# Optimization experiments

Measured on AMD Instinct MI355X. Metric: run time of the kernel, lower is better.

## Reference

```python
import jax, jax.numpy as jnp
import numpy as np
from jax import lax

TAU = 2.0      # LIF decay constant (source: tau = 2.0)
V_TH = 1.0     # spikingjelly LIFNode default threshold
ALPHA = 2.0    # ATan surrogate default alpha
BN_EPS = 1e-5


@jax.custom_vjp
def spike(v):
    # Heaviside with ATan surrogate gradient (spikingjelly surrogate.ATan)
    return (v >= V_TH).astype(v.dtype)

def _spike_fwd(v):
    return spike(v), v

def _spike_bwd(v, g):
    x = (jnp.pi / 2.0) * ALPHA * (v - V_TH)
    return (g * (ALPHA / 2.0) / (1.0 + x * x),)

spike.defvjp(_spike_fwd, _spike_bwd)


def lif_step(v, x):
    # leaky integrate: v += (x - (v - v_reset)) / tau, v_reset = 0
    v = v + (x - v) / TAU
    s = spike(v)
    # hard reset to 0; detach_reset=True -> stop_gradient on s in the reset path
    v = v * (1.0 - lax.stop_gradient(s))
    return v, s


def multistep_lif(x_seq):
    # x_seq: (T, ...) ; membrane state carried across T, initial v = 0
    v0 = jnp.zeros_like(x_seq[0])
    _, s_seq = lax.scan(lif_step, v0, x_seq)
    return s_seq


def setup_inputs() -> dict:
    key = jax.random.key(0)
    ks = jax.random.split(key, 3)
    bs, length, c_num, hidden = 64, 128, 32, 256
    x = jax.random.normal(ks[0], (bs, length, c_num), dtype=jnp.float32)
    conv_w = jax.random.normal(ks[1], (hidden, 1, 1, 3), dtype=jnp.float32) * 0.3
    conv_b = jnp.zeros((hidden,), jnp.float32)
    bn_gamma = jnp.ones((hidden,), jnp.float32)
    bn_beta = jnp.zeros((hidden,), jnp.float32)
    bn_mean = jnp.zeros((hidden,), jnp.float32)
    bn_var = jnp.ones((hidden,), jnp.float32)
    lin_w = jax.random.normal(ks[2], (hidden, hidden), dtype=jnp.float32) * (1.0 / np.sqrt(hidden))
    lin_b = jnp.zeros((hidden,), jnp.float32)
    return {"x": x, "conv_w": conv_w, "conv_b": conv_b, "bn_gamma": bn_gamma,
            "bn_beta": bn_beta, "bn_mean": bn_mean, "bn_var": bn_var,
            "lin_w": lin_w, "lin_b": lin_b}


def reference(x, conv_w, conv_b, bn_gamma, bn_beta, bn_mean, bn_var, lin_w, lin_b):
    bs, length, c_num = x.shape
    hidden = conv_w.shape[0]

    # ---- ConvEncoder ----
    xi = jnp.transpose(x, (0, 2, 1))[:, None]  # (bs, 1, c_num, length)
    enc = lax.conv_general_dilated(
        xi, conv_w, window_strides=(1, 1), padding=((0, 0), (1, 1)),
        dimension_numbers=("NCHW", "OIHW", "NCHW"))
    enc = enc + conv_b[None, :, None, None]
    # BatchNorm2d (eval mode, running stats)
    inv = bn_gamma * lax.rsqrt(bn_var + BN_EPS)
    enc = (enc - bn_mean[None, :, None, None]) * inv[None, :, None, None] + bn_beta[None, :, None, None]
    # multi-step LIF over channel dim T = hidden (as in source permute(1,0,2,3))
    enc = jnp.transpose(enc, (1, 0, 2, 3))          # (hidden, bs, c_num, length)
    spks_enc = multistep_lif(enc)                   # (hidden, bs, c_num, length)

    # ---- reshape to per-(bs*c_num) sequences of length `length` with feature hidden ----
    h = jnp.transpose(spks_enc, (1, 2, 3, 0)).reshape(bs * c_num, length, hidden)

    # ---- SpikeRNNCell recurrence over time (Linear + stateful LIF) ----
    def rnn_step(v, x_t):                           # x_t: (N, hidden)
        z = x_t @ lin_w.T + lin_b
        v = v + (z - v) / TAU
        s = spike(v)
        v = v * (1.0 - lax.stop_gradient(s))
        return v, s

    v0 = jnp.zeros((bs * c_num, hidden), x.dtype)
    _, s_seq = lax.scan(rnn_step, v0, jnp.transpose(h, (1, 0, 2)))  # (length, N, hidden)
    spks = s_seq[-1]                                # final-step spikes (N, hidden)

    spks = spks.reshape(bs, c_num * hidden, -1)     # (bs, c_num*hidden, 1)
    return jnp.transpose(spks, (0, 2, 1)), spks[:, :, -1]
```

## Files before the change

kernel.cpp:

```cpp
#include <hip/hip_runtime.h>
#include <stdint.h>

typedef unsigned short u16;
typedef unsigned int u32;
typedef unsigned long long u64;
typedef unsigned char u8;

typedef __attribute__((ext_vector_type(4))) int   i32x4;
typedef __attribute__((ext_vector_type(8))) int   i32x8;
typedef __attribute__((ext_vector_type(4))) float f32x4;
typedef __attribute__((ext_vector_type(2))) float f32x2;

#define OFF_WQ4  0u
#define WQ4_BYTES (2u * 32768u)
#define OFF_SCL  (OFF_WQ4 + WQ4_BYTES)

__device__ __forceinline__ f32x2 pk_fma(f32x2 a, f32x2 b, f32x2 c) {
    f32x2 d;
    asm("v_pk_fma_f32 %0, %1, %2, %3"
        : "=v"(d) : "v"(a), "v"(b), "v"(c));
    return d;
}
__device__ __forceinline__ f32x2 pk_fma_lw(f32x2 a, f32x2 b) {
    f32x2 d;
    asm("v_pk_fma_f32 %0, %1, %2, %1 op_sel:[0,0,1] op_sel_hi:[0,1,1]"
        : "=v"(d) : "v"(a), "v"(b));
    return d;
}
__device__ __forceinline__ f32x2 pk_fma_b11(f32x2 a, f32x2 b, f32x2 c) {
    f32x2 d;
    asm("v_pk_fma_f32 %0, %1, %2, %3 op_sel:[1,0,0] op_sel_hi:[1,1,1]"
        : "=v"(d) : "v"(a), "v"(b), "v"(c));
    return d;
}
__device__ __forceinline__ f32x2 pk_fma_b00(f32x2 a, f32x2 b, f32x2 c) {
    f32x2 d;
    asm("v_pk_fma_f32 %0, %1, %2, %3 op_sel:[0,0,0] op_sel_hi:[0,1,1]"
        : "=v"(d) : "v"(a), "v"(b), "v"(c));
    return d;
}

__device__ __forceinline__ u32 nib_perm(u32 byte) {
    u32 t1 = byte | (byte << 6);
    u32 t2 = t1 | (t1 << 12);
    u32 sel = t2 & 0x03030303u;
    return __builtin_amdgcn_perm(0x22200200u, 0x22200200u, sel);
}

__global__ __launch_bounds__(256) void prep_kernel(
    const float* __restrict__ lin_w, uint8_t* __restrict__ ws) {
    __shared__ float red[256];
    __shared__ u8 nib[256];
    int j = blockIdx.x, k = threadIdx.x;
    float wv = lin_w[j * 256 + k];
    red[k] = fabsf(wv);
    __syncthreads();
    #pragma unroll
    for (int s = 128; s > 0; s >>= 1) {
        if (k < s) red[k] = fmaxf(red[k], red[k + s]);
        __syncthreads();
    }
    float m = red[0];
    float S = (m > 0.f) ? 6.0f / m : 0.f;
    float v6 = wv * S;
    float av = fabsf(v6);
    int code;
    if      (av < 0.25f) code = 0;
    else if (av < 0.75f) code = 1;
    else if (av < 1.25f) code = 2;
    else if (av < 1.75f) code = 3;
    else if (av < 2.5f)  code = 4;
    else if (av < 3.5f)  code = 5;
    else if (av < 5.0f)  code = 6;
    else                 code = 7;
    nib[k] = (u8)(((v6 < 0.f && code) ? 8 : 0) | code);
    __syncthreads();
    if (k < 128) {
        u8 byte = (u8)(nib[2 * k] | (nib[2 * k + 1] << 4));
        int ks = k >> 6, kb = (k >> 4) & 3, bi = k & 15;
        (ws + OFF_WQ4)[ks * 32768 + (j * 4 + kb) * 16 + bi] = byte;
    }
    if (k == 0) ((float*)(ws + OFF_SCL))[j] = m * (1.0f / 12.0f);
}

__global__ __launch_bounds__(256, 2) void enc_gemm_kernel(
    const float* __restrict__ x,
    const float* __restrict__ conv_w, const float* __restrict__ conv_b,
    const float* __restrict__ gamma,  const float* __restrict__ beta,
    const float* __restrict__ mean,   const float* __restrict__ var,
    const uint4* __restrict__ wq4,
    const float* __restrict__ lin_b,  const float* __restrict__ sclp,
    float* __restrict__ out) {
    __shared__ __align__(16) uint8_t smem[57344];
    u32*   bits = (u32*)smem;
    f32x4* cfl  = (f32x4*)(smem + 16384);

    int tid  = threadIdx.x;
    int blk  = blockIdx.x;
    int lane = tid & 63;
    int w    = tid >> 6;
    int l15  = lane & 15;
    int quad = lane >> 4;
    int lb   = w * 256 + l15 * 4 + quad;

    float bias = lin_b[tid];
    float zscg = fmaxf(sclp[tid], 1e-37f);
    float uth  = (1.0f - bias) / zscg;
    float urst = (0.0f - bias) / zscg;

    i32x4 bb[2][4];
    #pragma unroll
    for (int ks = 0; ks < 2; ++ks)
        #pragma unroll
        for (int nf = 0; nf < 4; ++nf)
            bb[ks][nf] = ((const i32x4*)wq4)[(size_t)(ks * 2048 + nf * 64 + lb)];

    {
        int h = tid;
        float inv = gamma[h] / sqrtf(var[h] + 1e-5f);
        float K = (conv_b[h] - mean[h]) * inv + beta[h];
        f32x4 cc = {conv_w[h * 3 + 0] * inv * 0.5f,
                    conv_w[h * 3 + 1] * inv * 0.5f,
                    conv_w[h * 3 + 2] * inv * 0.5f, K * 0.5f};
        cfl[h] = cc;
    }

    int l     = tid & 127;
    int chalf = tid >> 7;
    int cpair = (blk * 2) & 31;
    int c     = cpair + chalf;
    int b0    = blk >> 4;
    int xb = b0 * 4096 + l * 32 + c;
    float xb0 = x[xb],            xb1 = x[xb + 131072];
    float xa0 = (l > 0)   ? x[xb - 32]          : 0.f;
    float xa1 = (l > 0)   ? x[xb + 131072 - 32] : 0.f;
    float xc0 = (l < 127) ? x[xb + 32]          : 0.f;
    float xc1 = (l < 127) ? x[xb + 131072 + 32] : 0.f;
    u32* d0 = bits + chalf * 1024 + l;
    u32* d1 = d0 + 2 * 1024;

    f32x2 XA = {xa0, xa1};
    f32x2 XB = {xb0, xb1};
    f32x2 XC = {xc0, xc1};
    const f32x2 hf2 = {0.5f, 0.5f};

    __syncthreads();
    f32x2 v2 = {0.f, 0.f};
    #pragma unroll 1
    for (int hc = 0; hc < 8; ++hc) {
        u32 c0 = 0, c1 = 0;
        #pragma unroll
        for (int k = 0; k < 32; ++k) {
            f32x4 a4 = cfl[hc * 32 + k];
            f32x2 p0 = __builtin_shufflevector(a4, a4, 0, 1);
            f32x2 p1 = __builtin_shufflevector(a4, a4, 2, 3);
            f32x2 e = pk_fma_lw(p1, XC);
            e = pk_fma_b11(p0, XB, e);
            e = pk_fma_b00(p0, XA, e);
            v2 = pk_fma(hf2, v2, e);
            bool s0 = (v2.x >= 1.0f);
            bool s1 = (v2.y >= 1.0f);
            c0 = (c0 << 1) | (u32)s0;
            c1 = (c1 << 1) | (u32)s1;
            v2.x = s0 ? 0.f : v2.x;
            v2.y = s1 ? 0.f : v2.y;
        }
        d0[hc * 128] = __builtin_bitreverse32(c0);
        d1[hc * 128] = __builtin_bitreverse32(c1);
    }

    __syncthreads();

    float* ZW = (float*)(smem + 20480 + (size_t)w * 9216);
    const u32* bp = bits + quad * 128 + l15;

    #pragma unroll 1
    for (int s = 0; s < 4; ++s) {
        int n = b0 * 32 + cpair + (s & 1) + (s >> 1) * 1024;

        u32 aw[8][2];
        #pragma unroll
        for (int mf = 0; mf < 8; ++mf)
            #pragma unroll
            for (int ks = 0; ks < 2; ++ks)
                aw[mf][ks] = bp[s * 1024 + ks * 512 + mf * 16];

        f32x4 acc[8][4];
        #pragma unroll
        for (int mf = 0; mf < 8; ++mf)
            #pragma unroll
            for (int nf = 0; nf < 4; ++nf) {
                f32x4 z = {0.f, 0.f, 0.f, 0.f};
                acc[mf][nf] = z;
            }

        i32x8 afr;
        afr[4] = 0; afr[5] = 0; afr[6] = 0; afr[7] = 0;

        #pragma unroll
        for (int ks = 0; ks < 2; ++ks) {
            i32x8 bfr[4];
            #pragma unroll
            for (int nf = 0; nf < 4; ++nf) {
                bfr[nf][0] = bb[ks][nf][0]; bfr[nf][1] = bb[ks][nf][1];
                bfr[nf][2] = bb[ks][nf][2]; bfr[nf][3] = bb[ks][nf][3];
                bfr[nf][4] = 0; bfr[nf][5] = 0; bfr[nf][6] = 0; bfr[nf][7] = 0;
            }
            #pragma unroll
            for (int mf = 0; mf < 8; ++mf) {
                u32 wbits = aw[mf][ks];
                afr[0] = (int)nib_perm(wbits & 0xFFu);
                afr[1] = (int)nib_perm((wbits >> 8) & 0xFFu);
                afr[2] = (int)nib_perm((wbits >> 16) & 0xFFu);
                afr[3] = (int)nib_perm(wbits >> 24);
                #pragma unroll
                for (int nf = 0; nf < 4; ++nf) {
                    acc[mf][nf] =
                        __builtin_amdgcn_mfma_scale_f32_16x16x128_f8f6f4(
                            afr, bfr[nf], acc[mf][nf], 4, 4,
                            0, 0x7F7F7F7F, 0, 0x7F7F7F7F);
                }
            }
        }

        float u = urst, sOut = 0.f;
        #pragma unroll
        for (int ph = 0; ph < 4; ++ph) {
            #pragma unroll
            for (int mm = 0; mm < 2; ++mm) {
                int mf = ph * 2 + mm;
                #pragma unroll
                for (int nf = 0; nf < 4; ++nf)
                    *(f32x4*)(ZW + (nf * 16 + l15) * 36 + mm * 16 + quad * 4) =
                        acc[mf][nf];
            }
            #pragma unroll
            for (int g = 0; g < 8; ++g) {
                f32x4 z4 = *(const f32x4*)(ZW + lane * 36 + g * 4);
                #pragma unroll
                for (int r = 0; r < 4; ++r) {
                    u = fmaf(0.5f, u, z4[r]);
                    bool sp = (u >= uth);
                    if (ph == 3 && g == 7 && r == 3) sOut = sp ? 1.f : 0.f;
                    u = sp ? urst : u;
                }
            }
        }
        out[(size_t)n * 256 + tid]           = sOut;
        out[524288u + (size_t)n * 256 + tid] = sOut;
    }
}

extern "C" void kernel_launch(void* const* d_in, const int* in_sizes, int n_in,
                              void* d_out, int out_size, void* d_ws, size_t ws_size,
                              hipStream_t stream) {
    const float* x      = (const float*)d_in[0];
    const float* conv_w = (const float*)d_in[1];
    const float* conv_b = (const float*)d_in[2];
    const float* gamma  = (const float*)d_in[3];
    const float* beta   = (const float*)d_in[4];
    const float* mean   = (const float*)d_in[5];
    const float* var    = (const float*)d_in[6];
    const float* lin_w  = (const float*)d_in[7];
    const float* lin_b  = (const float*)d_in[8];
    uint8_t* ws = (uint8_t*)d_ws;
    float* out = (float*)d_out;

    hipLaunchKernelGGL(prep_kernel, dim3(256), dim3(256), 0, stream,
                       lin_w, ws);
    hipLaunchKernelGGL(enc_gemm_kernel, dim3(512), dim3(256), 0, stream,
                       x, conv_w, conv_b, gamma, beta, mean, var,
                       (const uint4*)(ws + OFF_WQ4), lin_b,
                       (const float*)(ws + OFF_SCL), out);
}
```

Before: 107.7 us.

## Double block size and split MFMA rows across thread halves with LDS handoff

Launches 512 threads per block instead of 256, so each thread runs one scalar encoder LIF chain in place of a packed pair, and the two thread halves each compute half of the MFMA row fragments. The 256 scan threads then consume the results from two swizzled LDS ping-pong buffers across several barriers. Weight fragments are reloaded from global memory inside the loop instead of being held in registers. The intent is more wave-level parallelism and fewer registers per thread. In exchange, LDS rises to 80 KB, half the threads sit idle during the serial scan, and extra __syncthreads are added.

```diff
diff --git a/kernel.cpp b/kernel.cpp
--- a/kernel.cpp
+++ b/kernel.cpp
@@ -9,36 +9,10 @@
 typedef __attribute__((ext_vector_type(4))) int   i32x4;
 typedef __attribute__((ext_vector_type(8))) int   i32x8;
 typedef __attribute__((ext_vector_type(4))) float f32x4;
-typedef __attribute__((ext_vector_type(2))) float f32x2;
 
 #define OFF_WQ4  0u
 #define WQ4_BYTES (2u * 32768u)
 #define OFF_SCL  (OFF_WQ4 + WQ4_BYTES)
-
-__device__ __forceinline__ f32x2 pk_fma(f32x2 a, f32x2 b, f32x2 c) {
-    f32x2 d;
-    asm("v_pk_fma_f32 %0, %1, %2, %3"
-        : "=v"(d) : "v"(a), "v"(b), "v"(c));
-    return d;
-}
-__device__ __forceinline__ f32x2 pk_fma_lw(f32x2 a, f32x2 b) {
-    f32x2 d;
-    asm("v_pk_fma_f32 %0, %1, %2, %1 op_sel:[0,0,1] op_sel_hi:[0,1,1]"
-        : "=v"(d) : "v"(a), "v"(b));
-    return d;
-}
-__device__ __forceinline__ f32x2 pk_fma_b11(f32x2 a, f32x2 b, f32x2 c) {
-    f32x2 d;
-    asm("v_pk_fma_f32 %0, %1, %2, %3 op_sel:[1,0,0] op_sel_hi:[1,1,1]"
-        : "=v"(d) : "v"(a), "v"(b), "v"(c));
-    return d;
-}
-__device__ __forceinline__ f32x2 pk_fma_b00(f32x2 a, f32x2 b, f32x2 c) {
-    f32x2 d;
-    asm("v_pk_fma_f32 %0, %1, %2, %3 op_sel:[0,0,0] op_sel_hi:[0,1,1]"
-        : "=v"(d) : "v"(a), "v"(b), "v"(c));
-    return d;
-}
 
 __device__ __forceinline__ u32 nib_perm(u32 byte) {
     u32 t1 = byte | (byte << 6);
@@ -83,7 +57,26 @@
     if (k == 0) ((float*)(ws + OFF_SCL))[j] = m * (1.0f / 12.0f);
 }
 
-__global__ __launch_bounds__(256, 2) void enc_gemm_kernel(
+#define PHW(BUF, MB)                                                     \
+    _Pragma("unroll") for (int mm = 0; mm < 2; ++mm) {                   \
+        int co = ((mm << 4) | (quad << 2)) ^ lx4;                        \
+        _Pragma("unroll") for (int nf = 0; nf < 4; ++nf)                 \
+            *(f32x4*)((BUF) + (jq * 64 + nf * 16 + l15) * 32 + co) =     \
+                acc[(MB) + mm][nf];                                      \
+    }
+
+#define SCAN(BUF, LAST)                                                  \
+    _Pragma("unroll") for (int g = 0; g < 8; ++g) {                      \
+        f32x4 z4 = *(const f32x4*)((BUF) + tid * 32 + ((g << 2) ^ lx4)); \
+        _Pragma("unroll") for (int r = 0; r < 4; ++r) {                  \
+            u = fmaf(0.5f, u, z4[r]);                                    \
+            bool sp = (u >= uth);                                        \
+            if ((LAST) && g == 7 && r == 3) sOut = sp ? 1.f : 0.f;       \
+            u = sp ? urst : u;                                           \
+        }                                                                \
+    }
+
+__global__ __launch_bounds__(512, 4) void enc_gemm_kernel(
     const float* __restrict__ x,
     const float* __restrict__ conv_w, const float* __restrict__ conv_b,
     const float* __restrict__ gamma,  const float* __restrict__ beta,
@@ -91,31 +84,33 @@
     const uint4* __restrict__ wq4,
     const float* __restrict__ lin_b,  const float* __restrict__ sclp,
     float* __restrict__ out) {
-    __shared__ __align__(16) uint8_t smem[57344];
+    __shared__ __align__(16) uint8_t smem[81920];
     u32*   bits = (u32*)smem;
     f32x4* cfl  = (f32x4*)(smem + 16384);
+    float* bufA = (float*)(smem + 16384);
+    float* bufB = (float*)(smem + 49152);
 
     int tid  = threadIdx.x;
     int blk  = blockIdx.x;
     int lane = tid & 63;
     int w    = tid >> 6;
+    int th   = w >> 2;
+    int jq   = w & 3;
     int l15  = lane & 15;
     int quad = lane >> 4;
-    int lb   = w * 256 + l15 * 4 + quad;
-
-    float bias = lin_b[tid];
-    float zscg = fmaxf(sclp[tid], 1e-37f);
-    float uth  = (1.0f - bias) / zscg;
-    float urst = (0.0f - bias) / zscg;
-
-    i32x4 bb[2][4];
-    #pragma unroll
-    for (int ks = 0; ks < 2; ++ks)
-        #pragma unroll
-        for (int nf = 0; nf < 4; ++nf)
-            bb[ks][nf] = ((const i32x4*)wq4)[(size_t)(ks * 2048 + nf * 64 + lb)];
-
-    {
+    int lx4  = (lane & 7) << 2;
+    int b0   = blk >> 4;
+    int cpair = (blk & 15) * 2;
+
+    float uth = 0.f, urst = 0.f;
+    if (tid < 256) {
+        float bias = lin_b[tid];
+        float zscg = fmaxf(sclp[tid], 1e-37f);
+        uth  = (1.0f - bias) / zscg;
+        urst = (0.0f - bias) / zscg;
+    }
+
+    if (tid < 256) {
         int h = tid;
         float inv = gamma[h] / sqrtf(var[h] + 1e-5f);
         float K = (conv_b[h] - mean[h]) * inv + beta[h];
@@ -125,69 +120,52 @@
         cfl[h] = cc;
     }
 
-    int l     = tid & 127;
-    int chalf = tid >> 7;
-    int cpair = (blk * 2) & 31;
-    int c     = cpair + chalf;
-    int b0    = blk >> 4;
-    int xb = b0 * 4096 + l * 32 + c;
-    float xb0 = x[xb],            xb1 = x[xb + 131072];
-    float xa0 = (l > 0)   ? x[xb - 32]          : 0.f;
-    float xa1 = (l > 0)   ? x[xb + 131072 - 32] : 0.f;
-    float xc0 = (l < 127) ? x[xb + 32]          : 0.f;
-    float xc1 = (l < 127) ? x[xb + 131072 + 32] : 0.f;
-    u32* d0 = bits + chalf * 1024 + l;
-    u32* d1 = d0 + 2 * 1024;
-
-    f32x2 XA = {xa0, xa1};
-    f32x2 XB = {xb0, xb1};
-    f32x2 XC = {xc0, xc1};
-    const f32x2 hf2 = {0.5f, 0.5f};
-
-    __syncthreads();
-    f32x2 v2 = {0.f, 0.f};
-    #pragma unroll 1
-    for (int hc = 0; hc < 8; ++hc) {
-        u32 c0 = 0, c1 = 0;
-        #pragma unroll
-        for (int k = 0; k < 32; ++k) {
-            f32x4 a4 = cfl[hc * 32 + k];
-            f32x2 p0 = __builtin_shufflevector(a4, a4, 0, 1);
-            f32x2 p1 = __builtin_shufflevector(a4, a4, 2, 3);
-            f32x2 e = pk_fma_lw(p1, XC);
-            e = pk_fma_b11(p0, XB, e);
-            e = pk_fma_b00(p0, XA, e);
-            v2 = pk_fma(hf2, v2, e);
-            bool s0 = (v2.x >= 1.0f);
-            bool s1 = (v2.y >= 1.0f);
-            c0 = (c0 << 1) | (u32)s0;
-            c1 = (c1 << 1) | (u32)s1;
-            v2.x = s0 ? 0.f : v2.x;
-            v2.y = s1 ? 0.f : v2.y;
+    int l  = tid & 127;
+    int ch = (tid >> 7) & 1;
+    int bh = tid >> 8;
+    int xb = b0 * 4096 + l * 32 + cpair + ch + bh * 131072;
+    float xbv = x[xb];
+    float xav = (l > 0)   ? x[xb - 32] : 0.f;
+    float xcv = (l < 127) ? x[xb + 32] : 0.f;
+    u32* dst = bits + (bh * 2 + ch) * 1024 + l;
+
+    __syncthreads();
+    {
+        float v = 0.f;
+        #pragma unroll 1
+        for (int hc = 0; hc < 8; ++hc) {
+            u32 cc = 0;
+            #pragma unroll
+            for (int k = 0; k < 32; ++k) {
+                f32x4 a4 = cfl[hc * 32 + k];
+                float e = fmaf(a4[2], xcv, a4[3]);
+                e = fmaf(a4[1], xbv, e);
+                e = fmaf(a4[0], xav, e);
+                v = fmaf(0.5f, v, e);
+                bool sp = (v >= 1.0f);
+                cc = (cc << 1) | (u32)sp;
+                v = sp ? 0.f : v;
+            }
+            dst[hc * 128] = __builtin_bitreverse32(cc);
         }
-        d0[hc * 128] = __builtin_bitreverse32(c0);
-        d1[hc * 128] = __builtin_bitreverse32(c1);
-    }
-
-    __syncthreads();
-
-    float* ZW = (float*)(smem + 20480 + (size_t)w * 9216);
-    const u32* bp = bits + quad * 128 + l15;
+    }
+    __syncthreads();
+
+    int lb = jq * 256 + l15 * 4 + quad;
+    const u32* bp = bits + quad * 128 + th * 64 + l15;
 
     #pragma unroll 1
     for (int s = 0; s < 4; ++s) {
-        int n = b0 * 32 + cpair + (s & 1) + (s >> 1) * 1024;
-
-        u32 aw[8][2];
+        u32 aw[4][2];
         #pragma unroll
-        for (int mf = 0; mf < 8; ++mf)
+        for (int mf = 0; mf < 4; ++mf)
             #pragma unroll
             for (int ks = 0; ks < 2; ++ks)
                 aw[mf][ks] = bp[s * 1024 + ks * 512 + mf * 16];
 
-        f32x4 acc[8][4];
+        f32x4 acc[4][4];
         #pragma unroll
-        for (int mf = 0; mf < 8; ++mf)
+        for (int mf = 0; mf < 4; ++mf)
             #pragma unroll
             for (int nf = 0; nf < 4; ++nf) {
                 f32x4 z = {0.f, 0.f, 0.f, 0.f};
@@ -202,17 +180,18 @@
             i32x8 bfr[4];
             #pragma unroll
             for (int nf = 0; nf < 4; ++nf) {
-                bfr[nf][0] = bb[ks][nf][0]; bfr[nf][1] = bb[ks][nf][1];
-                bfr[nf][2] = bb[ks][nf][2]; bfr[nf][3] = bb[ks][nf][3];
+                i32x4 bv = ((const i32x4*)wq4)[(size_t)(ks * 2048 + nf * 64 + lb)];
+                bfr[nf][0] = bv[0]; bfr[nf][1] = bv[1];
+                bfr[nf][2] = bv[2]; bfr[nf][3] = bv[3];
                 bfr[nf][4] = 0; bfr[nf][5] = 0; bfr[nf][6] = 0; bfr[nf][7] = 0;
             }
             #pragma unroll
-            for (int mf = 0; mf < 8; ++mf) {
-                u32 wbits = aw[mf][ks];
-                afr[0] = (int)nib_perm(wbits & 0xFFu);
-                afr[1] = (int)nib_perm((wbits >> 8) & 0xFFu);
-                afr[2] = (int)nib_perm((wbits >> 16) & 0xFFu);
-                afr[3] = (int)nib_perm(wbits >> 24);
+            for (int mf = 0; mf < 4; ++mf) {
+                u32 wb = aw[mf][ks];
+                afr[0] = (int)nib_perm(wb & 0xFFu);
+                afr[1] = (int)nib_perm((wb >> 8) & 0xFFu);
+                afr[2] = (int)nib_perm((wb >> 16) & 0xFFu);
+                afr[3] = (int)nib_perm(wb >> 24);
                 #pragma unroll
                 for (int nf = 0; nf < 4; ++nf) {
                     acc[mf][nf] =
@@ -224,30 +203,23 @@
         }
 
         float u = urst, sOut = 0.f;
-        #pragma unroll
-        for (int ph = 0; ph < 4; ++ph) {
-            #pragma unroll
-            for (int mm = 0; mm < 2; ++mm) {
-                int mf = ph * 2 + mm;
-                #pragma unroll
-                for (int nf = 0; nf < 4; ++nf)
-                    *(f32x4*)(ZW + (nf * 16 + l15) * 36 + mm * 16 + quad * 4) =
-                        acc[mf][nf];
-            }
-            #pragma unroll
-            for (int g = 0; g < 8; ++g) {
-                f32x4 z4 = *(const f32x4*)(ZW + lane * 36 + g * 4);
-                #pragma unroll
-                for (int r = 0; r < 4; ++r) {
-                    u = fmaf(0.5f, u, z4[r]);
-                    bool sp = (u >= uth);
-                    if (ph == 3 && g == 7 && r == 3) sOut = sp ? 1.f : 0.f;
-                    u = sp ? urst : u;
-                }
-            }
+        if (th == 0) { PHW(bufA, 0) PHW(bufB, 2) }
+        __syncthreads();
+        if (tid < 256) { SCAN(bufA, 0) }
+        __syncthreads();
+        if (th == 1) { PHW(bufA, 0) }
+        if (tid < 256) { SCAN(bufB, 0) }
+        __syncthreads();
+        if (th == 1) { PHW(bufB, 2) }
+        if (tid < 256) { SCAN(bufA, 0) }
+        __syncthreads();
+        if (tid < 256) {
+            SCAN(bufB, 1)
+            int n = b0 * 32 + cpair + (s & 1) + (s >> 1) * 1024;
+            out[(size_t)n * 256 + tid]           = sOut;
+            out[524288u + (size_t)n * 256 + tid] = sOut;
         }
-        out[(size_t)n * 256 + tid]           = sOut;
-        out[524288u + (size_t)n * 256 + tid] = sOut;
+        __syncthreads();
     }
 }
 
@@ -268,7 +240,7 @@
 
     hipLaunchKernelGGL(prep_kernel, dim3(256), dim3(256), 0, stream,
                        lin_w, ws);
-    hipLaunchKernelGGL(enc_gemm_kernel, dim3(512), dim3(256), 0, stream,
+    hipLaunchKernelGGL(enc_gemm_kernel, dim3(512), dim3(512), 0, stream,
                        x, conv_w, conv_b, gamma, beta, mean, var,
                        (const uint4*)(ws + OFF_WQ4), lin_b,
                        (const float*)(ws + OFF_SCL), out);
```

New measurement: 113.1 us. +5.0%, slower.

## Halve per-block work to double grid and occupancy, swizzle staging buffer

Applied to the files above, without the earlier changes.

Each block now handles a single channel c instead of a channel pair, so the grid doubles to 1024 blocks and each block runs 2 GEMM/LIF sequences instead of 4. Shared memory drops to 40 KB and launch bounds request 4 blocks per CU to raise occupancy. The padded 36-stride ZW staging layout is replaced by an XOR-swizzled 32-stride layout to save LDS while avoiding bank conflicts. In exchange, only half the threads do the serial encoder LIF scan, the weight fragments are reloaded per block, and the tighter launch bound may force register spills.

```diff
diff --git a/kernel.cpp b/kernel.cpp
--- a/kernel.cpp
+++ b/kernel.cpp
@@ -83,7 +83,7 @@
     if (k == 0) ((float*)(ws + OFF_SCL))[j] = m * (1.0f / 12.0f);
 }
 
-__global__ __launch_bounds__(256, 2) void enc_gemm_kernel(
+__global__ __launch_bounds__(256, 4) void enc_gemm_kernel(
     const float* __restrict__ x,
     const float* __restrict__ conv_w, const float* __restrict__ conv_b,
     const float* __restrict__ gamma,  const float* __restrict__ beta,
@@ -91,9 +91,9 @@
     const uint4* __restrict__ wq4,
     const float* __restrict__ lin_b,  const float* __restrict__ sclp,
     float* __restrict__ out) {
-    __shared__ __align__(16) uint8_t smem[57344];
+    __shared__ __align__(16) uint8_t smem[40960];
     u32*   bits = (u32*)smem;
-    f32x4* cfl  = (f32x4*)(smem + 16384);
+    f32x4* cfl  = (f32x4*)(smem + 8192);
 
     int tid  = threadIdx.x;
     int blk  = blockIdx.x;
@@ -102,6 +102,8 @@
     int l15  = lane & 15;
     int quad = lane >> 4;
     int lb   = w * 256 + l15 * 4 + quad;
+    int b0   = blk >> 5;
+    int c    = blk & 31;
 
     float bias = lin_b[tid];
     float zscg = fmaxf(sclp[tid], 1e-37f);
@@ -124,60 +126,57 @@
                     conv_w[h * 3 + 2] * inv * 0.5f, K * 0.5f};
         cfl[h] = cc;
     }
-
-    int l     = tid & 127;
-    int chalf = tid >> 7;
-    int cpair = (blk * 2) & 31;
-    int c     = cpair + chalf;
-    int b0    = blk >> 4;
-    int xb = b0 * 4096 + l * 32 + c;
-    float xb0 = x[xb],            xb1 = x[xb + 131072];
-    float xa0 = (l > 0)   ? x[xb - 32]          : 0.f;
-    float xa1 = (l > 0)   ? x[xb + 131072 - 32] : 0.f;
-    float xc0 = (l < 127) ? x[xb + 32]          : 0.f;
-    float xc1 = (l < 127) ? x[xb + 131072 + 32] : 0.f;
-    u32* d0 = bits + chalf * 1024 + l;
-    u32* d1 = d0 + 2 * 1024;
-
-    f32x2 XA = {xa0, xa1};
-    f32x2 XB = {xb0, xb1};
-    f32x2 XC = {xc0, xc1};
-    const f32x2 hf2 = {0.5f, 0.5f};
-
-    __syncthreads();
-    f32x2 v2 = {0.f, 0.f};
+    __syncthreads();
+
+    if (tid < 128) {
+        int l  = tid;
+        int xb = b0 * 4096 + l * 32 + c;
+        float xb0 = x[xb],            xb1 = x[xb + 131072];
+        float xa0 = (l > 0)   ? x[xb - 32]          : 0.f;
+        float xa1 = (l > 0)   ? x[xb + 131072 - 32] : 0.f;
+        float xc0 = (l < 127) ? x[xb + 32]          : 0.f;
+        float xc1 = (l < 127) ? x[xb + 131072 + 32] : 0.f;
+        u32* d0 = bits + l;
+        u32* d1 = d0 + 1024;
+
+        f32x2 XA = {xa0, xa1};
+        f32x2 XB = {xb0, xb1};
+        f32x2 XC = {xc0, xc1};
+        const f32x2 hf2 = {0.5f, 0.5f};
+
+        f32x2 v2 = {0.f, 0.f};
+        #pragma unroll 1
+        for (int hc = 0; hc < 8; ++hc) {
+            u32 c0 = 0, c1 = 0;
+            #pragma unroll
+            for (int k = 0; k < 32; ++k) {
+                f32x4 a4 = cfl[hc * 32 + k];
+                f32x2 p0 = __builtin_shufflevector(a4, a4, 0, 1);
+                f32x2 p1 = __builtin_shufflevector(a4, a4, 2, 3);
+                f32x2 e = pk_fma_lw(p1, XC);
+                e = pk_fma_b11(p0, XB, e);
+                e = pk_fma_b00(p0, XA, e);
+                v2 = pk_fma(hf2, v2, e);
+                bool s0 = (v2.x >= 1.0f);
+                bool s1 = (v2.y >= 1.0f);
+                c0 = (c0 << 1) | (u32)s0;
+                c1 = (c1 << 1) | (u32)s1;
+                v2.x = s0 ? 0.f : v2.x;
+                v2.y = s1 ? 0.f : v2.y;
+            }
+            d0[hc * 128] = __builtin_bitreverse32(c0);
+            d1[hc * 128] = __builtin_bitreverse32(c1);
+        }
+    }
+    __syncthreads();
+
+    float* ZW = (float*)(smem + 8192 + (size_t)w * 8192);
+    const u32* bp = bits + quad * 128 + l15;
+    int wswz = (l15 & 7) << 2;
+    int rswz = (lane & 7) << 2;
+
     #pragma unroll 1
-    for (int hc = 0; hc < 8; ++hc) {
-        u32 c0 = 0, c1 = 0;
-        #pragma unroll
-        for (int k = 0; k < 32; ++k) {
-            f32x4 a4 = cfl[hc * 32 + k];
-            f32x2 p0 = __builtin_shufflevector(a4, a4, 0, 1);
-            f32x2 p1 = __builtin_shufflevector(a4, a4, 2, 3);
-            f32x2 e = pk_fma_lw(p1, XC);
-            e = pk_fma_b11(p0, XB, e);
-            e = pk_fma_b00(p0, XA, e);
-            v2 = pk_fma(hf2, v2, e);
-            bool s0 = (v2.x >= 1.0f);
-            bool s1 = (v2.y >= 1.0f);
-            c0 = (c0 << 1) | (u32)s0;
-            c1 = (c1 << 1) | (u32)s1;
-            v2.x = s0 ? 0.f : v2.x;
-            v2.y = s1 ? 0.f : v2.y;
-        }
-        d0[hc * 128] = __builtin_bitreverse32(c0);
-        d1[hc * 128] = __builtin_bitreverse32(c1);
-    }
-
-    __syncthreads();
-
-    float* ZW = (float*)(smem + 20480 + (size_t)w * 9216);
-    const u32* bp = bits + quad * 128 + l15;
-
-    #pragma unroll 1
-    for (int s = 0; s < 4; ++s) {
-        int n = b0 * 32 + cpair + (s & 1) + (s >> 1) * 1024;
-
+    for (int s = 0; s < 2; ++s) {
         u32 aw[8][2];
         #pragma unroll
         for (int mf = 0; mf < 8; ++mf)
@@ -208,11 +207,11 @@
             }
             #pragma unroll
             for (int mf = 0; mf < 8; ++mf) {
-                u32 wbits = aw[mf][ks];
-                afr[0] = (int)nib_perm(wbits & 0xFFu);
-                afr[1] = (int)nib_perm((wbits >> 8) & 0xFFu);
-                afr[2] = (int)nib_perm((wbits >> 16) & 0xFFu);
-                afr[3] = (int)nib_perm(wbits >> 24);
+                u32 wb = aw[mf][ks];
+                afr[0] = (int)nib_perm(wb & 0xFFu);
+                afr[1] = (int)nib_perm((wb >> 8) & 0xFFu);
+                afr[2] = (int)nib_perm((wb >> 16) & 0xFFu);
+                afr[3] = (int)nib_perm(wb >> 24);
                 #pragma unroll
                 for (int nf = 0; nf < 4; ++nf) {
                     acc[mf][nf] =
@@ -229,14 +228,14 @@
             #pragma unroll
             for (int mm = 0; mm < 2; ++mm) {
                 int mf = ph * 2 + mm;
+                int col = ((mm << 4) | (quad << 2)) ^ wswz;
                 #pragma unroll
                 for (int nf = 0; nf < 4; ++nf)
-                    *(f32x4*)(ZW + (nf * 16 + l15) * 36 + mm * 16 + quad * 4) =
-                        acc[mf][nf];
+                    *(f32x4*)(ZW + (nf * 16 + l15) * 32 + col) = acc[mf][nf];
             }
             #pragma unroll
             for (int g = 0; g < 8; ++g) {
-                f32x4 z4 = *(const f32x4*)(ZW + lane * 36 + g * 4);
+                f32x4 z4 = *(const f32x4*)(ZW + lane * 32 + ((g << 2) ^ rswz));
                 #pragma unroll
                 for (int r = 0; r < 4; ++r) {
                     u = fmaf(0.5f, u, z4[r]);
@@ -246,6 +245,7 @@
                 }
             }
         }
+        int n = b0 * 32 + c + s * 1024;
         out[(size_t)n * 256 + tid]           = sOut;
         out[524288u + (size_t)n * 256 + tid] = sOut;
     }
@@ -268,7 +268,7 @@
 
     hipLaunchKernelGGL(prep_kernel, dim3(256), dim3(256), 0, stream,
                        lin_w, ws);
-    hipLaunchKernelGGL(enc_gemm_kernel, dim3(512), dim3(256), 0, stream,
+    hipLaunchKernelGGL(enc_gemm_kernel, dim3(1024), dim3(256), 0, stream,
                        x, conv_w, conv_b, gamma, beta, mean, var,
                        (const uint4*)(ws + OFF_WQ4), lin_b,
                        (const float*)(ws + OFF_SCL), out);
```

Result: slower. 150.4 us (+39.7%).
